# Performance work log

Hardware: AMD Instinct MI355X
Metric: run time of the kernel (lower is better)

## Reference

```python
import jax, jax.numpy as jnp
import numpy as np

N = 50000
E = 800000
D_IN = 128
D_HID = 128
D_OUT = 128
EPS = 1e-5


def setup_inputs() -> dict:
    key = jax.random.key(0)
    ks = jax.random.split(key, 10)
    x = jax.random.normal(ks[0], (N, D_IN), dtype=jnp.float32)
    edge_index = jax.random.randint(ks[1], (2, E), 0, N, dtype=jnp.int64)
    def lin(k, fi, fo):
        return jax.random.normal(k, (fi, fo), dtype=jnp.float32) / jnp.sqrt(jnp.float32(fi))
    return {
        "x": x,
        "edge_index": edge_index,
        "W1": lin(ks[2], D_IN, D_HID), "b1": jnp.zeros((D_HID,), jnp.float32),
        "W2": lin(ks[3], D_HID, D_HID), "b2": jnp.zeros((D_HID,), jnp.float32),
        "W3": lin(ks[4], D_HID, D_OUT), "b3": jnp.zeros((D_OUT,), jnp.float32),
        "g1": jnp.ones((D_HID,), jnp.float32), "be1": jnp.zeros((D_HID,), jnp.float32),
        "g2": jnp.ones((D_HID,), jnp.float32), "be2": jnp.zeros((D_HID,), jnp.float32),
    }


def _gcn_conv(x, src, dst, norm, W, b):
    # x' = D^{-1/2}(A+I)D^{-1/2} X W + b  (PyG GCNConv with self-loops)
    h = x @ W                              # [N, F]
    msgs = h[src] * norm[:, None]          # [E+N, F] gather
    agg = jax.ops.segment_sum(msgs, dst, num_segments=x.shape[0])  # scatter-add
    return agg + b


def _batchnorm(x, gamma, beta):
    mu = jnp.mean(x, axis=0)
    var = jnp.mean((x - mu) ** 2, axis=0)  # biased var, as in torch BN
    return (x - mu) * jax.lax.rsqrt(var + EPS) * gamma + beta


def reference(x, edge_index, W1, b1, W2, b2, W3, b3, g1, be1, g2, be2):
    n = x.shape[0]
    loops = jnp.arange(n, dtype=edge_index.dtype)
    src = jnp.concatenate([edge_index[0], loops])
    dst = jnp.concatenate([edge_index[1], loops])
    deg = jax.ops.segment_sum(jnp.ones_like(dst, dtype=x.dtype), dst, num_segments=n)
    dinv = jnp.where(deg > 0, jax.lax.rsqrt(deg), 0.0)
    norm = dinv[src] * dinv[dst]           # [E+N]

    h = _gcn_conv(x, src, dst, norm, W1, b1)
    h = jax.nn.relu(_batchnorm(h, g1, be1))
    h = _gcn_conv(h, src, dst, norm, W2, b2)
    h = jax.nn.relu(_batchnorm(h, g2, be2))
    h = _gcn_conv(h, src, dst, norm, W3, b3)
    # F.normalize(p=2, dim=-1)
    return h / jnp.maximum(jnp.linalg.norm(h, axis=-1, keepdims=True), 1e-12)
```

## Files before the change

### kernel.cpp

```cpp
#include <hip/hip_runtime.h>
#include <hip/hip_bf16.h>

#define D 128

typedef __bf16 bf16x8 __attribute__((ext_vector_type(8)));
typedef float floatx4 __attribute__((ext_vector_type(4)));


__global__ void k_count(const int* __restrict__ dst, int E, int* __restrict__ cnt) {
    int e = blockIdx.x * blockDim.x + threadIdx.x;
    if (e < E) atomicAdd(&cnt[dst[e]], 1);
}

__global__ __launch_bounds__(256) void k_scan1(const int* __restrict__ cnt, int n,
                                               int* __restrict__ bsum) {
    int i = blockIdx.x * 256 + threadIdx.x;
    int x = (i < n) ? cnt[i] : 0;
    #pragma unroll
    for (int off = 32; off > 0; off >>= 1) x += __shfl_xor(x, off, 64);
    __shared__ int ws[4];
    if ((threadIdx.x & 63) == 0) ws[threadIdx.x >> 6] = x;
    __syncthreads();
    if (threadIdx.x == 0) bsum[blockIdx.x] = ws[0] + ws[1] + ws[2] + ws[3];
}

__global__ __launch_bounds__(256) void k_scan3(const int* __restrict__ cnt,
                                               const int* __restrict__ bsum, int n, int E,
                                               int* __restrict__ row_ptr, int* __restrict__ cursor,
                                               float* __restrict__ dinv) {
    __shared__ int ws[4];
    int t = threadIdx.x;
    int lane = t & 63, wid = t >> 6;
    int xb = 0;
    for (int j = t; j < blockIdx.x; j += 256) xb += bsum[j];
    #pragma unroll
    for (int off = 32; off > 0; off >>= 1) xb += __shfl_xor(xb, off, 64);
    if (lane == 0) ws[wid] = xb;
    __syncthreads();
    int o = ws[0] + ws[1] + ws[2] + ws[3];
    __syncthreads();
    int i = blockIdx.x * 256 + t;
    int x = (i < n) ? cnt[i] : 0;
    int incl = x;
    #pragma unroll
    for (int off = 1; off < 64; off <<= 1) {
        int y = __shfl_up(incl, off, 64);
        if (lane >= off) incl += y;
    }
    if (lane == 63) ws[wid] = incl;
    __syncthreads();
    for (int w = 0; w < wid; w++) o += ws[w];
    if (i < n) {
        int excl = o + incl - x;
        row_ptr[i] = excl;
        cursor[i] = excl;
        dinv[i] = rsqrtf((float)(x + 1));
    }
    if (blockIdx.x == 0 && t == 0) row_ptr[n] = E;
}

__global__ __launch_bounds__(256) void k_fill(const int* __restrict__ src,
                                              const int* __restrict__ dst, int E,
                                              int* __restrict__ cursor,
                                              unsigned short* __restrict__ esrc, int n) {
    int range = blockIdx.x & 7;
    int rb = blockIdx.x >> 3;
    int nb = gridDim.x >> 3;
    int rs = (n + 7) >> 3;
    int lo = range * rs, hi = lo + rs;
    int step = nb * 256;
    for (int e = rb * 256 + threadIdx.x; e < E; e += step) {
        int d = dst[e];
        int s = src[e];
        if (d >= lo && d < hi) {
            int p = atomicAdd(&cursor[d], 1);
            esrc[p] = (unsigned short)s;
        }
    }
}


__global__ __launch_bounds__(256) void k_prepw(const float* __restrict__ W1,
                                               const float* __restrict__ W2,
                                               const float* __restrict__ W3,
                                               unsigned short* __restrict__ Wt,
                                               int* __restrict__ cnt, int n) {
    int b = blockIdx.x;
    if (b < 3) {
        const float* W = (b == 0) ? W1 : (b == 1) ? W2 : W3;
        unsigned short* o = Wt + b * 16384;
        for (int i = threadIdx.x; i < 16384; i += 256) {
            int k = i >> 7, nn = i & 127;
            __hip_bfloat16 h = __float2bfloat16(W[i]);
            o[nn * 128 + k] = *(unsigned short*)&h;
        }
    } else {
        int i = (b - 3) * 256 + threadIdx.x;
        if (i < n) cnt[i] = 0;
    }
}


__global__ __launch_bounds__(256) void k_gemm(
    const float* __restrict__ X, const unsigned short* __restrict__ Wt,
    const float* __restrict__ scale, const float* __restrict__ stats_in,
    const float* __restrict__ gamma, const float* __restrict__ beta,
    float* __restrict__ stats_zero,
    unsigned* __restrict__ hs, int n, float invN) {
    __shared__ unsigned short Wl[128 * 128];
    __shared__ float bnl[256];
    int t = threadIdx.x;
    if (stats_in && t < 128) {
        float s = stats_in[t] + stats_in[256 + t] + stats_in[512 + t] + stats_in[768 + t];
        float q = stats_in[128 + t] + stats_in[384 + t] + stats_in[640 + t] + stats_in[896 + t];
        float mean = s * invN;
        float var = q * invN - mean * mean;
        float a = gamma[t] * rsqrtf(var + 1e-5f);
        bnl[t] = a;
        bnl[128 + t] = beta[t] - mean * a;
    }
    if (stats_zero && blockIdx.x == 0) {
        stats_zero[t] = 0.f;
        stats_zero[256 + t] = 0.f;
        stats_zero[512 + t] = 0.f;
        stats_zero[768 + t] = 0.f;
    }
    {
        const uint4* wg = (const uint4*)Wt;
        uint4* wl4 = (uint4*)Wl;
        #pragma unroll
        for (int j = 0; j < 8; j++) {
            int idx = j * 256 + t;
            int nn = idx >> 4, lc = idx & 15;
            wl4[nn * 16 + (lc ^ (nn & 15))] = wg[idx];
        }
    }
    __syncthreads();

    int l = t & 63, w = t >> 6;
    int lm = l & 15, quad = l >> 4;
    int m = blockIdx.x * 64 + w * 16 + lm;
    int rm = (m < n) ? m : (n - 1);
    const float* xrow = X + (size_t)rm * D;

    floatx4 acc[8];
    #pragma unroll
    for (int nt = 0; nt < 8; nt++) acc[nt] = (floatx4){0.f, 0.f, 0.f, 0.f};

    #pragma unroll
    for (int ks = 0; ks < 4; ks++) {
        int k0 = ks * 32 + quad * 8;
        float4 xa = *(const float4*)(xrow + k0);
        float4 xb = *(const float4*)(xrow + k0 + 4);
        if (stats_in) {
            float4 a0 = *(const float4*)&bnl[k0];
            float4 a1 = *(const float4*)&bnl[k0 + 4];
            float4 c0 = *(const float4*)&bnl[128 + k0];
            float4 c1 = *(const float4*)&bnl[128 + k0 + 4];
            xa.x = fmaxf(xa.x * a0.x + c0.x, 0.f);
            xa.y = fmaxf(xa.y * a0.y + c0.y, 0.f);
            xa.z = fmaxf(xa.z * a0.z + c0.z, 0.f);
            xa.w = fmaxf(xa.w * a0.w + c0.w, 0.f);
            xb.x = fmaxf(xb.x * a1.x + c1.x, 0.f);
            xb.y = fmaxf(xb.y * a1.y + c1.y, 0.f);
            xb.z = fmaxf(xb.z * a1.z + c1.z, 0.f);
            xb.w = fmaxf(xb.w * a1.w + c1.w, 0.f);
        }
        bf16x8 xf;
        xf[0] = (__bf16)xa.x; xf[1] = (__bf16)xa.y;
        xf[2] = (__bf16)xa.z; xf[3] = (__bf16)xa.w;
        xf[4] = (__bf16)xb.x; xf[5] = (__bf16)xb.y;
        xf[6] = (__bf16)xb.z; xf[7] = (__bf16)xb.w;
        int pc = (ks * 4 + quad) ^ lm;
        #pragma unroll
        for (int nt = 0; nt < 8; nt++) {
            const bf16x8 wf = *(const bf16x8*)&Wl[(nt * 16 + lm) * 128 + pc * 8];
            acc[nt] = __builtin_amdgcn_mfma_f32_16x16x32_bf16(wf, xf, acc[nt], 0, 0, 0);
        }
    }

    float s = scale[rm];
    if (m < n) {
        #pragma unroll
        for (int nt = 0; nt < 8; nt++) {
            __hip_bfloat16 h0 = __float2bfloat16(acc[nt][0] * s);
            __hip_bfloat16 h1 = __float2bfloat16(acc[nt][1] * s);
            __hip_bfloat16 h2 = __float2bfloat16(acc[nt][2] * s);
            __hip_bfloat16 h3 = __float2bfloat16(acc[nt][3] * s);
            uint2 uu;
            uu.x = (unsigned)*(unsigned short*)&h0 | ((unsigned)*(unsigned short*)&h1 << 16);
            uu.y = (unsigned)*(unsigned short*)&h2 | ((unsigned)*(unsigned short*)&h3 << 16);
            *(uint2*)&hs[((size_t)(nt >> 1) * n + m) * 16 + (nt & 1) * 8 + quad * 2] = uu;
        }
    }
}


__device__ inline float2 bf2f(unsigned u) {
    union { unsigned i; float f; } lo, hi;
    lo.i = u << 16;
    hi.i = u & 0xffff0000u;
    float2 r; r.x = lo.f; r.y = hi.f; return r;
}

__device__ __forceinline__ void agg_node_w(
    const unsigned* __restrict__ hsp, const unsigned short* __restrict__ esrc,
    float* __restrict__ out, float (*lsS)[32], float (*lsQ)[32],
    int node, int beg, int end, int e_cur, uint4 sv, float sc,
    float4 bA, float4 bB, int grp, int sub, int qd, int qe, int p, int mode) {
    float2 a0 = bf2f(qd == 0 ? sv.x : 0u);
    float2 a1 = bf2f(qd == 0 ? sv.y : 0u);
    float2 a2 = bf2f(qd == 0 ? sv.z : 0u);
    float2 a3 = bf2f(qd == 0 ? sv.w : 0u);

    for (int base = beg; base < end; base += 16) {
        int mm = end - base;
        if (mm > 16) mm = 16;
        int e_nxt = (base + 16 + sub < end) ? (int)esrc[base + 16 + sub] : 0;
        int u0, u1, u2, u3;
        float w0, w1, w2, w3;
        {
            int ei = qd;
            int ix = ei < mm ? ei : mm - 1;
            u0 = __shfl(e_cur, ix, 16);
            w0 = ei < mm ? 1.f : 0.f;
        }
        {
            int ei = 4 + qd;
            int ix = ei < mm ? ei : mm - 1;
            u1 = __shfl(e_cur, ix, 16);
            w1 = ei < mm ? 1.f : 0.f;
        }
        {
            int ei = 8 + qd;
            int ix = ei < mm ? ei : mm - 1;
            u2 = __shfl(e_cur, ix, 16);
            w2 = ei < mm ? 1.f : 0.f;
        }
        {
            int ei = 12 + qd;
            int ix = ei < mm ? ei : mm - 1;
            u3 = __shfl(e_cur, ix, 16);
            w3 = ei < mm ? 1.f : 0.f;
        }
        uint4 g0 = *(const uint4*)&hsp[(size_t)u0 * 16 + qe * 4];
        uint4 g1 = *(const uint4*)&hsp[(size_t)u1 * 16 + qe * 4];
        uint4 g2 = *(const uint4*)&hsp[(size_t)u2 * 16 + qe * 4];
        uint4 g3 = *(const uint4*)&hsp[(size_t)u3 * 16 + qe * 4];
        float2 v;
        v = bf2f(g0.x); a0.x = fmaf(v.x, w0, a0.x); a0.y = fmaf(v.y, w0, a0.y);
        v = bf2f(g0.y); a1.x = fmaf(v.x, w0, a1.x); a1.y = fmaf(v.y, w0, a1.y);
        v = bf2f(g0.z); a2.x = fmaf(v.x, w0, a2.x); a2.y = fmaf(v.y, w0, a2.y);
        v = bf2f(g0.w); a3.x = fmaf(v.x, w0, a3.x); a3.y = fmaf(v.y, w0, a3.y);
        v = bf2f(g1.x); a0.x = fmaf(v.x, w1, a0.x); a0.y = fmaf(v.y, w1, a0.y);
        v = bf2f(g1.y); a1.x = fmaf(v.x, w1, a1.x); a1.y = fmaf(v.y, w1, a1.y);
        v = bf2f(g1.z); a2.x = fmaf(v.x, w1, a2.x); a2.y = fmaf(v.y, w1, a2.y);
        v = bf2f(g1.w); a3.x = fmaf(v.x, w1, a3.x); a3.y = fmaf(v.y, w1, a3.y);
        v = bf2f(g2.x); a0.x = fmaf(v.x, w2, a0.x); a0.y = fmaf(v.y, w2, a0.y);
        v = bf2f(g2.y); a1.x = fmaf(v.x, w2, a1.x); a1.y = fmaf(v.y, w2, a1.y);
        v = bf2f(g2.z); a2.x = fmaf(v.x, w2, a2.x); a2.y = fmaf(v.y, w2, a2.y);
        v = bf2f(g2.w); a3.x = fmaf(v.x, w2, a3.x); a3.y = fmaf(v.y, w2, a3.y);
        v = bf2f(g3.x); a0.x = fmaf(v.x, w3, a0.x); a0.y = fmaf(v.y, w3, a0.y);
        v = bf2f(g3.y); a1.x = fmaf(v.x, w3, a1.x); a1.y = fmaf(v.y, w3, a1.y);
        v = bf2f(g3.z); a2.x = fmaf(v.x, w3, a2.x); a2.y = fmaf(v.y, w3, a2.y);
        v = bf2f(g3.w); a3.x = fmaf(v.x, w3, a3.x); a3.y = fmaf(v.y, w3, a3.y);
        e_cur = e_nxt;
    }

    a0.x += __shfl_xor(a0.x, 4, 16); a0.x += __shfl_xor(a0.x, 8, 16);
    a0.y += __shfl_xor(a0.y, 4, 16); a0.y += __shfl_xor(a0.y, 8, 16);
    a1.x += __shfl_xor(a1.x, 4, 16); a1.x += __shfl_xor(a1.x, 8, 16);
    a1.y += __shfl_xor(a1.y, 4, 16); a1.y += __shfl_xor(a1.y, 8, 16);
    a2.x += __shfl_xor(a2.x, 4, 16); a2.x += __shfl_xor(a2.x, 8, 16);
    a2.y += __shfl_xor(a2.y, 4, 16); a2.y += __shfl_xor(a2.y, 8, 16);
    a3.x += __shfl_xor(a3.x, 4, 16); a3.x += __shfl_xor(a3.x, 8, 16);
    a3.y += __shfl_xor(a3.y, 4, 16); a3.y += __shfl_xor(a3.y, 8, 16);

    if (qd == 0) {
        float4 r0, r1;
        r0.x = fmaf(a0.x, sc, bA.x);
        r0.y = fmaf(a0.y, sc, bA.y);
        r0.z = fmaf(a1.x, sc, bA.z);
        r0.w = fmaf(a1.y, sc, bA.w);
        r1.x = fmaf(a2.x, sc, bB.x);
        r1.y = fmaf(a2.y, sc, bB.y);
        r1.z = fmaf(a3.x, sc, bB.z);
        r1.w = fmaf(a3.y, sc, bB.w);
        float* op = &out[(size_t)node * D + p * 32 + qe * 8];
        *(float4*)op = r0;
        *(float4*)(op + 4) = r1;
        if (mode == 0) {
            lsS[grp][qe * 8 + 0] += r0.x; lsQ[grp][qe * 8 + 0] += r0.x * r0.x;
            lsS[grp][qe * 8 + 1] += r0.y; lsQ[grp][qe * 8 + 1] += r0.y * r0.y;
            lsS[grp][qe * 8 + 2] += r0.z; lsQ[grp][qe * 8 + 2] += r0.z * r0.z;
            lsS[grp][qe * 8 + 3] += r0.w; lsQ[grp][qe * 8 + 3] += r0.w * r0.w;
            lsS[grp][qe * 8 + 4] += r1.x; lsQ[grp][qe * 8 + 4] += r1.x * r1.x;
            lsS[grp][qe * 8 + 5] += r1.y; lsQ[grp][qe * 8 + 5] += r1.y * r1.y;
            lsS[grp][qe * 8 + 6] += r1.z; lsQ[grp][qe * 8 + 6] += r1.z * r1.z;
            lsS[grp][qe * 8 + 7] += r1.w; lsQ[grp][qe * 8 + 7] += r1.w * r1.w;
        }
    }
}

__global__ __launch_bounds__(256) void k_agg(
    const unsigned* __restrict__ hs, const int* __restrict__ row_ptr,
    const unsigned short* __restrict__ esrc, const float* __restrict__ dinv,
    const float* __restrict__ bias, float* __restrict__ out,
    float* __restrict__ stats4, int n, int mode) {
    __shared__ float lsS[16][32];
    __shared__ float lsQ[16][32];
    int t = threadIdx.x;
    int grp = t >> 4, sub = t & 15;
    int qd = sub >> 2;
    int qe = sub & 3;
    int bid = blockIdx.x;
    int p = (bid >> 1) & 3;
    int nblk = (bid >> 3) * 2 + (bid & 1);
    const unsigned* hsp = hs + (size_t)p * n * 16;

    lsS[t >> 5][t & 31] = 0.f;
    lsS[(t >> 5) + 8][t & 31] = 0.f;
    lsQ[t >> 5][t & 31] = 0.f;
    lsQ[(t >> 5) + 8][t & 31] = 0.f;
    __syncthreads();

    float4 bA = *(const float4*)&bias[p * 32 + qe * 8];
    float4 bB = *(const float4*)&bias[p * 32 + qe * 8 + 4];

    int node0 = nblk * 32 + grp * 2;
    int rp[3];
    #pragma unroll
    for (int k = 0; k < 3; k++) {
        int ik = node0 + k;
        if (ik > n) ik = n;
        rp[k] = row_ptr[ik];
    }

    int eC[2];
    uint4 svC[2];
    float dvC[2];
    #pragma unroll
    for (int k = 0; k < 2; k++) {
        int nk = node0 + k;
        int ck = nk < n ? nk : n - 1;
        eC[k] = (rp[k] + sub < rp[k + 1]) ? (int)esrc[rp[k] + sub] : 0;
        svC[k] = *(const uint4*)&hsp[(size_t)ck * 16 + qe * 4];
        dvC[k] = dinv[ck];
    }

    #pragma unroll
    for (int ni = 0; ni < 2; ni++) {
        int node = node0 + ni;
        if (node >= n) break;
        agg_node_w(hsp, esrc, out, lsS, lsQ, node, rp[ni], rp[ni + 1], eC[ni],
                   svC[ni], dvC[ni], bA, bB, grp, sub, qd, qe, p, mode);
    }

    if (mode == 0) {
        __syncthreads();
        if (t < 32) {
            float a = 0.f, c = 0.f;
            for (int g = 0; g < 16; g++) {
                a += lsS[g][t];
                c += lsQ[g][t];
            }
            float* sbuf = stats4 + ((bid >> 2) & 3) * 256;
            atomicAdd(&sbuf[p * 32 + t], a);
            atomicAdd(&sbuf[128 + p * 32 + t], c);
        }
    }
}


__global__ __launch_bounds__(256) void k_l2norm(const float* __restrict__ h,
                                                float* __restrict__ out, int n) {
    int node = blockIdx.x * 4 + (threadIdx.x >> 6);
    if (node >= n) return;
    int lane = threadIdx.x & 63;
    float2 v = *(const float2*)&h[(size_t)node * D + lane * 2];
    float pw = v.x * v.x + v.y * v.y;
    #pragma unroll
    for (int off = 32; off > 0; off >>= 1) pw += __shfl_xor(pw, off, 64);
    float sc = 1.0f / fmaxf(sqrtf(pw), 1e-12f);
    float2 r;
    r.x = v.x * sc;
    r.y = v.y * sc;
    *(float2*)&out[(size_t)node * D + lane * 2] = r;
}


extern "C" void kernel_launch(void* const* d_in, const int* in_sizes, int n_in,
                              void* d_out, int out_size, void* d_ws, size_t ws_size,
                              hipStream_t stream) {
    const float* x  = (const float*)d_in[0];
    const int*   ei = (const int*)d_in[1];
    const float* W1 = (const float*)d_in[2];
    const float* b1 = (const float*)d_in[3];
    const float* W2 = (const float*)d_in[4];
    const float* b2 = (const float*)d_in[5];
    const float* W3 = (const float*)d_in[6];
    const float* b3 = (const float*)d_in[7];
    const float* g1 = (const float*)d_in[8];
    const float* be1 = (const float*)d_in[9];
    const float* g2 = (const float*)d_in[10];
    const float* be2 = (const float*)d_in[11];

    const int N = in_sizes[0] / D;
    const int E = in_sizes[1] / 2;
    const int* src = ei;
    const int* dst = ei + E;
    const float invN = 1.0f / (float)N;

    float* Y       = (float*)d_ws;
    unsigned short* hs = (unsigned short*)(Y + (size_t)N * D);
    float* dinv    = (float*)(hs + (size_t)N * D);
    float* statsA  = dinv + N;
    float* statsB  = statsA + 1024;
    unsigned short* wt = (unsigned short*)(statsB + 1024);
    int*   cnt     = (int*)(wt + 3 * 16384);
    int*   row_ptr = cnt + N;
    int*   cursor  = row_ptr + N + 1;
    int*   bsum    = cursor + N;
    unsigned short* esrc = (unsigned short*)(bsum + 256);

    const int TB = 256;
    const int gE = (E + TB - 1) / TB;
    const int NB = (N + 255) / 256;
    const int gGemm = (N + 63) / 64;
    dim3 gFill(896);
    const int gx = (N + 31) / 32;
    const int gxp = (gx + 1) & ~1;
    dim3 gAgg(gxp * 4);
    const int gNode = (N + 3) / 4;

    k_prepw<<<3 + NB, TB, 0, stream>>>(W1, W2, W3, wt, cnt, N);
    k_count<<<gE, TB, 0, stream>>>(dst, E, cnt);
    k_scan1<<<NB, TB, 0, stream>>>(cnt, N, bsum);
    k_scan3<<<NB, TB, 0, stream>>>(cnt, bsum, N, E, row_ptr, cursor, dinv);
    k_fill<<<gFill, TB, 0, stream>>>(src, dst, E, cursor, esrc, N);

    k_gemm<<<gGemm, TB, 0, stream>>>(x, wt, dinv, nullptr, nullptr, nullptr, statsA,
                                     (unsigned*)hs, N, invN);
    k_agg<<<gAgg, TB, 0, stream>>>((const unsigned*)hs, row_ptr, esrc, dinv, b1, Y,
                                   statsA, N, 0);

    k_gemm<<<gGemm, TB, 0, stream>>>(Y, wt + 16384, dinv, statsA, g1, be1, statsB,
                                     (unsigned*)hs, N, invN);
    k_agg<<<gAgg, TB, 0, stream>>>((const unsigned*)hs, row_ptr, esrc, dinv, b2, Y,
                                   statsB, N, 0);

    k_gemm<<<gGemm, TB, 0, stream>>>(Y, wt + 32768, dinv, statsB, g2, be2, nullptr,
                                     (unsigned*)hs, N, invN);
    k_agg<<<gAgg, TB, 0, stream>>>((const unsigned*)hs, row_ptr, esrc, dinv, b3, Y,
                                   nullptr, N, 1);
    k_l2norm<<<gNode, TB, 0, stream>>>(Y, (float*)d_out, N);
}
```

Measured before the change: 327.7 us.

## Sort nodes by in-degree buckets to balance aggregation work across wavefronts

Adds a degree histogram in the scan kernel, a bucket prefix kernel, and a placement kernel that builds a permutation of nodes ordered by descending in-degree. The aggregation kernel then processes nodes in that permuted order, so nodes of similar degree share a wavefront and block and divergence is reduced. The cost is two extra small launches, an indirection through perm, and scattered output writes and row_ptr reads instead of sequential ones.

```diff
diff --git a/kernel.cpp b/kernel.cpp
--- a/kernel.cpp
+++ b/kernel.cpp
@@ -27,7 +27,8 @@
 __global__ __launch_bounds__(256) void k_scan3(const int* __restrict__ cnt,
                                                const int* __restrict__ bsum, int n, int E,
                                                int* __restrict__ row_ptr, int* __restrict__ cursor,
-                                               float* __restrict__ dinv) {
+                                               float* __restrict__ dinv,
+                                               int* __restrict__ bcnt) {
     __shared__ int ws[4];
     int t = threadIdx.x;
     int lane = t & 63, wid = t >> 6;
@@ -55,8 +56,44 @@
         row_ptr[i] = excl;
         cursor[i] = excl;
         dinv[i] = rsqrtf((float)(x + 1));
+        atomicAdd(&bcnt[x < 63 ? x : 63], 1);
     }
     if (blockIdx.x == 0 && t == 0) row_ptr[n] = E;
+}
+
+__global__ void k_bprefix(const int* __restrict__ bcnt, int* __restrict__ boff,
+                          int* __restrict__ bcur) {
+    if (threadIdx.x == 0) {
+        int acc = 0;
+        for (int b = 63; b >= 0; b--) {
+            boff[b] = acc;
+            acc += bcnt[b];
+        }
+    }
+    __syncthreads();
+    if (threadIdx.x < 64) bcur[threadIdx.x] = boff[threadIdx.x];
+}
+
+__global__ __launch_bounds__(256) void k_place(const int* __restrict__ cnt,
+                                               const int* __restrict__ boff,
+                                               int* __restrict__ bcur,
+                                               unsigned short* __restrict__ perm, int n) {
+    __shared__ int hist[64];
+    __shared__ int base[64];
+    int t = threadIdx.x;
+    if (t < 64) hist[t] = 0;
+    __syncthreads();
+    int i = blockIdx.x * 256 + t;
+    int b = 0, rank = 0;
+    if (i < n) {
+        int x = cnt[i];
+        b = x < 63 ? x : 63;
+        rank = atomicAdd(&hist[b], 1);
+    }
+    __syncthreads();
+    if (t < 64 && hist[t] > 0) base[t] = atomicAdd(&bcur[t], hist[t]);
+    __syncthreads();
+    if (i < n) perm[base[b] + rank] = (unsigned short)i;
 }
 
 __global__ __launch_bounds__(256) void k_fill(const int* __restrict__ src,
@@ -84,7 +121,8 @@
                                                const float* __restrict__ W2,
                                                const float* __restrict__ W3,
                                                unsigned short* __restrict__ Wt,
-                                               int* __restrict__ cnt, int n) {
+                                               int* __restrict__ cnt,
+                                               int* __restrict__ bcnt, int n) {
     int b = blockIdx.x;
     if (b < 3) {
         const float* W = (b == 0) ? W1 : (b == 1) ? W2 : W3;
@@ -95,6 +133,7 @@
             o[nn * 128 + k] = *(unsigned short*)&h;
         }
     } else {
+        if (b == 3 && threadIdx.x < 64) bcnt[threadIdx.x] = 0;
         int i = (b - 3) * 256 + threadIdx.x;
         if (i < n) cnt[i] = 0;
     }
@@ -305,6 +344,7 @@
 __global__ __launch_bounds__(256) void k_agg(
     const unsigned* __restrict__ hs, const int* __restrict__ row_ptr,
     const unsigned short* __restrict__ esrc, const float* __restrict__ dinv,
+    const unsigned short* __restrict__ perm,
     const float* __restrict__ bias, float* __restrict__ out,
     float* __restrict__ stats4, int n, int mode) {
     __shared__ float lsS[16][32];
@@ -327,13 +367,15 @@
     float4 bA = *(const float4*)&bias[p * 32 + qe * 8];
     float4 bB = *(const float4*)&bias[p * 32 + qe * 8 + 4];
 
-    int node0 = nblk * 32 + grp * 2;
-    int rp[3];
-    #pragma unroll
-    for (int k = 0; k < 3; k++) {
-        int ik = node0 + k;
-        if (ik > n) ik = n;
-        rp[k] = row_ptr[ik];
+    int j0 = nblk * 32 + grp * 2;
+    int pm[2];
+    pm[0] = (int)perm[j0 < n ? j0 : n - 1];
+    pm[1] = (int)perm[j0 + 1 < n ? j0 + 1 : n - 1];
+    int rpB[2], rpE[2];
+    #pragma unroll
+    for (int k = 0; k < 2; k++) {
+        rpB[k] = row_ptr[pm[k]];
+        rpE[k] = row_ptr[pm[k] + 1];
     }
 
     int eC[2];
@@ -341,18 +383,15 @@
     float dvC[2];
     #pragma unroll
     for (int k = 0; k < 2; k++) {
-        int nk = node0 + k;
-        int ck = nk < n ? nk : n - 1;
-        eC[k] = (rp[k] + sub < rp[k + 1]) ? (int)esrc[rp[k] + sub] : 0;
-        svC[k] = *(const uint4*)&hsp[(size_t)ck * 16 + qe * 4];
-        dvC[k] = dinv[ck];
+        eC[k] = (rpB[k] + sub < rpE[k]) ? (int)esrc[rpB[k] + sub] : 0;
+        svC[k] = *(const uint4*)&hsp[(size_t)pm[k] * 16 + qe * 4];
+        dvC[k] = dinv[pm[k]];
     }
 
     #pragma unroll
     for (int ni = 0; ni < 2; ni++) {
-        int node = node0 + ni;
-        if (node >= n) break;
-        agg_node_w(hsp, esrc, out, lsS, lsQ, node, rp[ni], rp[ni + 1], eC[ni],
+        if (j0 + ni >= n) break;
+        agg_node_w(hsp, esrc, out, lsS, lsQ, pm[ni], rpB[ni], rpE[ni], eC[ni],
                    svC[ni], dvC[ni], bA, bB, grp, sub, qd, qe, p, mode);
     }
 
@@ -421,7 +460,11 @@
     int*   row_ptr = cnt + N;
     int*   cursor  = row_ptr + N + 1;
     int*   bsum    = cursor + N;
-    unsigned short* esrc = (unsigned short*)(bsum + 256);
+    int*   bcnt    = bsum + 256;
+    int*   boff    = bcnt + 64;
+    int*   bcur    = boff + 64;
+    unsigned short* perm = (unsigned short*)(bcur + 64);
+    unsigned short* esrc = perm + ((N + 1) & ~1);
 
     const int TB = 256;
     const int gE = (E + TB - 1) / TB;
@@ -433,25 +476,27 @@
     dim3 gAgg(gxp * 4);
     const int gNode = (N + 3) / 4;
 
-    k_prepw<<<3 + NB, TB, 0, stream>>>(W1, W2, W3, wt, cnt, N);
+    k_prepw<<<3 + NB, TB, 0, stream>>>(W1, W2, W3, wt, cnt, bcnt, N);
     k_count<<<gE, TB, 0, stream>>>(dst, E, cnt);
     k_scan1<<<NB, TB, 0, stream>>>(cnt, N, bsum);
-    k_scan3<<<NB, TB, 0, stream>>>(cnt, bsum, N, E, row_ptr, cursor, dinv);
+    k_scan3<<<NB, TB, 0, stream>>>(cnt, bsum, N, E, row_ptr, cursor, dinv, bcnt);
+    k_bprefix<<<1, 64, 0, stream>>>(bcnt, boff, bcur);
+    k_place<<<NB, TB, 0, stream>>>(cnt, boff, bcur, perm, N);
     k_fill<<<gFill, TB, 0, stream>>>(src, dst, E, cursor, esrc, N);
 
     k_gemm<<<gGemm, TB, 0, stream>>>(x, wt, dinv, nullptr, nullptr, nullptr, statsA,
                                      (unsigned*)hs, N, invN);
-    k_agg<<<gAgg, TB, 0, stream>>>((const unsigned*)hs, row_ptr, esrc, dinv, b1, Y,
-                                   statsA, N, 0);
+    k_agg<<<gAgg, TB, 0, stream>>>((const unsigned*)hs, row_ptr, esrc, dinv, perm, b1,
+                                   Y, statsA, N, 0);
 
     k_gemm<<<gGemm, TB, 0, stream>>>(Y, wt + 16384, dinv, statsA, g1, be1, statsB,
                                      (unsigned*)hs, N, invN);
-    k_agg<<<gAgg, TB, 0, stream>>>((const unsigned*)hs, row_ptr, esrc, dinv, b2, Y,
-                                   statsB, N, 0);
+    k_agg<<<gAgg, TB, 0, stream>>>((const unsigned*)hs, row_ptr, esrc, dinv, perm, b2,
+                                   Y, statsB, N, 0);
 
     k_gemm<<<gGemm, TB, 0, stream>>>(Y, wt + 32768, dinv, statsB, g2, be2, nullptr,
                                      (unsigned*)hs, N, invN);
-    k_agg<<<gAgg, TB, 0, stream>>>((const unsigned*)hs, row_ptr, esrc, dinv, b3, Y,
-                                   nullptr, N, 1);
+    k_agg<<<gAgg, TB, 0, stream>>>((const unsigned*)hs, row_ptr, esrc, dinv, perm, b3,
+                                   Y, nullptr, N, 1);
     k_l2norm<<<gNode, TB, 0, stream>>>(Y, (float*)d_out, N);
 }
```

New measurement: 472.6 us. +44.2%, slower.
